# Optimization experiments

Hardware: AMD Instinct MI355X
Metric: run time of the kernel (lower is better)

## Reference

```python
import jax
import jax.numpy as jnp
from jax import lax
import numpy as np

# module hyperparameters (match init_kwargs)
IN_C, OUT_C = 32, 64
K, STRIDE, PAD, DIL = 3, 1, 1, 1
GRID_SIZE, ORDER = 5, 3
GRID_LO, GRID_HI = -1.0, 1.0
SCALE_SPLINE = 1.0
EPS = 1e-8


def _knot_grid():
    # grid = arange(-order, grid_size+order+1) * h + lo ; length = grid_size + 2*order + 1 = 12
    h = (GRID_HI - GRID_LO) / GRID_SIZE
    return jnp.arange(-ORDER, GRID_SIZE + ORDER + 1, dtype=jnp.float32) * h + GRID_LO


def _bspline_bases(x):
    """Cox-de Boor recursion. x: (N, P) -> bases: (N, P, GRID_SIZE+ORDER)."""
    grid = _knot_grid()
    xe = x[..., None]  # (N, P, 1)
    bases = ((xe >= grid[:-1]) & (xe < grid[1:])).astype(x.dtype)  # (N, P, 11)
    for k in range(1, ORDER + 1):
        left_den = jnp.maximum(grid[k:-1] - grid[:-(k + 1)], EPS)
        right_den = jnp.maximum(grid[k + 1:] - grid[1:-k], EPS)
        bases = ((xe - grid[:-(k + 1)]) / left_den * bases[..., :-1]
                 + (grid[k + 1:] - xe) / right_den * bases[..., 1:])
    return bases  # (N, P, 8)


def setup_inputs() -> dict:
    key = jax.random.key(0)
    k1, k2, k3 = jax.random.split(key, 3)
    x = jax.random.normal(k1, (4, IN_C, 56, 56), dtype=jnp.float32)
    base_weight = jax.random.normal(k2, (OUT_C, IN_C, K, K), dtype=jnp.float32) * 0.05
    spline_weight = jax.random.normal(k3, (OUT_C, IN_C * K * K, GRID_SIZE + ORDER), dtype=jnp.float32) * 0.05
    spline_scaler = jnp.ones((OUT_C,), dtype=jnp.float32)
    return {"x": x, "base_weight": base_weight,
            "spline_weight": spline_weight, "spline_scaler": spline_scaler}


def reference(x, base_weight, spline_weight, spline_scaler):
    B, C, H, W = x.shape
    pad = [(PAD, PAD), (PAD, PAD)]
    # base path: conv2d -> SiLU
    base_conv = lax.conv_general_dilated(
        x, base_weight, window_strides=(STRIDE, STRIDE), padding=pad,
        rhs_dilation=(DIL, DIL), dimension_numbers=("NCHW", "OIHW", "NCHW"))
    base_out = jax.nn.silu(base_conv)

    # unfold: (B, C*K*K, oh, ow) with torch Unfold channel ordering (c, kh, kw)
    patches = lax.conv_general_dilated_patches(
        x, filter_shape=(K, K), window_strides=(STRIDE, STRIDE), padding=pad,
        rhs_dilation=(DIL, DIL))
    oh, ow = patches.shape[2], patches.shape[3]
    num_patches = oh * ow
    # (B*num_patches, C*K*K)
    pf = patches.reshape(B, C * K * K, num_patches).transpose(0, 2, 1).reshape(-1, C * K * K)

    bases = _bspline_bases(pf)  # (N, P, F)
    # contract patch-dim and basis-dim against spline weights
    spl = jnp.einsum("npf,opf->no", bases, spline_weight) * spline_scaler  # (N, O)
    spl = spl.reshape(B, num_patches, OUT_C).transpose(0, 2, 1).reshape(B, OUT_C, oh, ow)
    return base_out + SCALE_SPLINE * spl
```

## Files before the change

### kernel.cpp

```cpp
#include <hip/hip_runtime.h>
#include <math.h>


typedef __attribute__((ext_vector_type(8))) short bf16x8;
typedef __attribute__((ext_vector_type(4))) float f32x4;
typedef __attribute__((ext_vector_type(16))) float f32x16;

#define MFMA32(a, b, c) __builtin_amdgcn_mfma_f32_32x32x16_bf16((a), (b), (c), 0, 0, 0)

__device__ __forceinline__ unsigned short f2bf(float f) {
    unsigned u = __builtin_bit_cast(unsigned, f);
    u = (u + 0x7fffu + ((u >> 16) & 1u)) >> 16;
    return (unsigned short)u;
}

__device__ __forceinline__ void eval_bases(float v, float bs[8]) {
    #pragma unroll
    for (int i = 0; i < 8; ++i) bs[i] = 0.0f;
    float t = (v + 2.2f) * 2.5f;
    if (t >= 0.0f && t < 11.0f) {
        int j = (int)t;
        if (j > 10) j = 10;
        float knot = (float)(j - 3) * 0.4f - 1.0f;
        float u  = (v - knot) * 2.5f;
        float um = 1.0f - u;
        float u2 = u * u, u3 = u2 * u;
        const float s6 = 1.0f / 6.0f;
        float w0 = um * um * um * s6;
        float w1 = (3.0f * u3 - 6.0f * u2 + 4.0f) * s6;
        float w2 = (-3.0f * u3 + 3.0f * u2 + 3.0f * u + 1.0f) * s6;
        float w3 = u3 * s6;
        int i0 = j - 3;
        if (i0 >= 0)               bs[i0]     = w0;
        if (i0 + 1 >= 0 && i0 < 7) bs[i0 + 1] = w1;
        if (i0 + 2 >= 0 && i0 < 6) bs[i0 + 2] = w2;
        if (i0 + 3 <= 7)           bs[i0 + 3] = w3;
    }
}

__global__ __launch_bounds__(256)
void cvt_swz_kernel(const float* __restrict__ ws, const float* __restrict__ wb,
                    unsigned short* __restrict__ wst, unsigned short* __restrict__ wbt) {
    int i = blockIdx.x * 256 + threadIdx.x;
    if (i < 147456) {
        int j = i & 7, l = (i >> 3) & 63, tq = i >> 9;
        int t = tq % 144, nqq = tq / 144;
        int oc = nqq * 32 + (l & 31);
        int k  = t * 16 + (l >> 5) * 8 + j;
        wst[i] = f2bf(ws[oc * 2304 + k]);
    } else {
        int i2 = i - 147456;
        if (i2 < 18432) {
            int j = i2 & 7, l = (i2 >> 3) & 63, tq = i2 >> 9;
            int t = tq % 18, nqq = tq / 18;
            int oc  = nqq * 32 + (l & 31);
            int tap = t >> 1;
            int c   = 16 * (t & 1) + (l >> 5) * 8 + j;
            wbt[i2] = f2bf(wb[oc * 288 + c * 9 + tap]);
        }
    }
}

__global__ __launch_bounds__(512)
void kan_mfma_kernel(const float* __restrict__ x,
                     const float* __restrict__ sc,
                     const unsigned short* __restrict__ wst,
                     const unsigned short* __restrict__ wbt,
                     float* __restrict__ out) {
    __shared__ unsigned short smem[29600];
    unsigned short* sb = smem;
    unsigned short* xh = smem + 25600;

    const int tid = threadIdx.x;
    const int bx  = blockIdx.x;
    const int b   = bx / 49;
    const int r   = bx - b * 49;
    const int ty  = r / 7;
    const int tx  = r - ty * 7;
    const int h0  = ty * 8, w0 = tx * 8;

    const int lane = tid & 63;
    const int wv   = tid >> 6;
    const int nqq  = wv & 1;
    const int kq   = wv >> 1;
    const int hl   = lane >> 5;
    const int rl   = lane & 31;
    const int py   = rl >> 3, px = rl & 7;

    float vv[7];
    #pragma unroll
    for (int j = 0; j < 7; ++j) {
        int i = tid + j * 512;
        float val = 0.0f;
        if (i < 3200) {
            int c  = i / 100;
            int hp = i - c * 100;
            int hy = hp / 10;
            int hx = hp - hy * 10;
            int hh = h0 + hy - 1, ww = w0 + hx - 1;
            if ((unsigned)hh < 56u && (unsigned)ww < 56u)
                val = x[((b * 32 + c) * 56 + hh) * 56 + ww];
        }
        vv[j] = val;
    }
    #pragma unroll
    for (int j = 0; j < 7; ++j) {
        int i = tid + j * 512;
        if (i < 3200) {
            int c  = i / 100;
            int hp = i - c * 100;
            float bs[8];
            eval_bases(vv[j], bs);
            bf16x8 pk;
            #pragma unroll
            for (int j2 = 0; j2 < 8; ++j2) pk[j2] = (short)f2bf(bs[j2]);
            *reinterpret_cast<bf16x8*>(&sb[i * 8]) = pk;
            xh[hp * 40 + c] = f2bf(vv[j]);
        }
    }
    __syncthreads();

    int aoff2[9];
    #pragma unroll
    for (int u = 0; u < 9; ++u) {
        int tt  = 2 * u + hl;
        int dc  = tt >= 9 ? 1 : 0;
        int tap = tt - 9 * dc;
        int th  = tap / 3;
        int tw  = tap - th * 3;
        aoff2[u] = (dc * 100 + (py + th) * 10 + (px + tw)) * 8;
    }

    f32x16 accS0 = {0,0,0,0,0,0,0,0,0,0,0,0,0,0,0,0};
    f32x16 accS1 = {0,0,0,0,0,0,0,0,0,0,0,0,0,0,0,0};

    const unsigned short* bp = wst + ((nqq * 144 + kq * 36) * 64 + lane) * 8;
    for (int a = 0; a < 4; ++a) {
        const int cbase = (kq * 8 + 2 * a) * 800;
        #pragma unroll
        for (int u = 0; u < 9; ++u) {
            bf16x8 bw = *reinterpret_cast<const bf16x8*>(bp + (a * 9 + u) * 512);
            bf16x8 a0 = *reinterpret_cast<const bf16x8*>(&sb[cbase + aoff2[u]]);
            bf16x8 a1 = *reinterpret_cast<const bf16x8*>(&sb[cbase + aoff2[u] + 320]);
            accS0 = MFMA32(a0, bw, accS0);
            accS1 = MFMA32(a1, bw, accS1);
        }
    }

    f32x16 accB0 = {0,0,0,0,0,0,0,0,0,0,0,0,0,0,0,0};
    f32x16 accB1 = {0,0,0,0,0,0,0,0,0,0,0,0,0,0,0,0};
    if (kq == 0) {
        const unsigned short* bbp = wbt + (nqq * 18 * 64 + lane) * 8;
        const int c0 = hl * 8;
        #pragma unroll
        for (int t = 0; t < 18; ++t) {
            const int tap = t >> 1, th = tap / 3, tw = tap - 3 * th;
            bf16x8 bw = *reinterpret_cast<const bf16x8*>(bbp + t * 512);
            int xa = ((py + th) * 10 + (px + tw)) * 40 + 16 * (t & 1) + c0;
            bf16x8 a0 = *reinterpret_cast<const bf16x8*>(&xh[xa]);
            bf16x8 a1 = *reinterpret_cast<const bf16x8*>(&xh[xa + 1600]);
            accB0 = MFMA32(a0, bw, accB0);
            accB1 = MFMA32(a1, bw, accB1);
        }
    }

    __syncthreads();
    float* red = reinterpret_cast<float*>(smem);
    const int col = nqq * 64 + lane;
    if (kq) {
        const int rb = (kq - 1) * 4096;
        #pragma unroll
        for (int w = 0; w < 16; ++w) red[rb + w * 128 + col] = accS0[w];
        #pragma unroll
        for (int w = 0; w < 16; ++w) red[rb + (16 + w) * 128 + col] = accS1[w];
    }
    __syncthreads();
    if (kq == 0) {
        #pragma unroll
        for (int rr = 0; rr < 3; ++rr) {
            const int rb = rr * 4096;
            #pragma unroll
            for (int w = 0; w < 16; ++w) accS0[w] += red[rb + w * 128 + col];
            #pragma unroll
            for (int w = 0; w < 16; ++w) accS1[w] += red[rb + (16 + w) * 128 + col];
        }

        const int oc  = nqq * 32 + rl;
        const float scv = sc[oc];
        #pragma unroll
        for (int mq = 0; mq < 2; ++mq) {
            f32x16 aS = mq ? accS1 : accS0;
            f32x16 aB = mq ? accB1 : accB0;
            #pragma unroll
            for (int q = 0; q < 4; ++q) {
                float* ob = out + ((b * 64 + oc) * 56 + h0 + mq * 4 + q) * 56 + w0 + 4 * hl;
                f32x4 res;
                #pragma unroll
                for (int rr = 0; rr < 4; ++rr) {
                    float bv = aB[q * 4 + rr];
                    float si = bv / (1.0f + __expf(-bv));
                    res[rr] = si + scv * aS[q * 4 + rr];
                }
                *reinterpret_cast<f32x4*>(ob) = res;
            }
        }
    }
}

extern "C" void kernel_launch(void* const* d_in, const int* in_sizes, int n_in,
                              void* d_out, int out_size, void* d_ws, size_t ws_size,
                              hipStream_t stream) {
    const float* x  = (const float*)d_in[0];
    const float* wb = (const float*)d_in[1];
    const float* ws = (const float*)d_in[2];
    const float* sc = (const float*)d_in[3];
    float* out = (float*)d_out;

    unsigned short* wst = (unsigned short*)d_ws;
    unsigned short* wbt = wst + 147456;

    cvt_swz_kernel<<<648, 256, 0, stream>>>(ws, wb, wst, wbt);
    kan_mfma_kernel<<<196, 512, 0, stream>>>(x, sc, wst, wbt, out);
}
```

Before: 76.83 us.

## Repartition warps into M-halves and K-halves, prefetch weights into registers

Warps now split the output tile by row-half (mh) and the reduction dimension into two halves (kh), instead of four K-quarters each holding two M-blocks. The base-conv MFMAs are spread over all warps rather than only the kq==0 group, and the LDS cross-warp reduction shrinks from three partials to one. Spline weight fragments are double-buffered in registers and base weights are loaded before the first barrier, so global loads overlap the basis evaluation and the MFMA work. The cost is higher register pressure from the 18-entry weight buffer, plus one extra exchanged accumulator for the base path.

```diff
diff --git a/kernel.cpp b/kernel.cpp
--- a/kernel.cpp
+++ b/kernel.cpp
@@ -82,10 +82,12 @@
     const int lane = tid & 63;
     const int wv   = tid >> 6;
     const int nqq  = wv & 1;
-    const int kq   = wv >> 1;
+    const int kh   = (wv >> 1) & 1;
+    const int mh   = wv >> 2;
+    const int rl   = lane & 31;
     const int hl   = lane >> 5;
-    const int rl   = lane & 31;
-    const int py   = rl >> 3, px = rl & 7;
+    const int py0  = (rl >> 3) + 4 * mh;
+    const int px0  = rl & 7;
 
     float vv[7];
     #pragma unroll
@@ -118,9 +120,24 @@
             xh[hp * 40 + c] = f2bf(vv[j]);
         }
     }
+
+    const unsigned short* bp = wst + ((nqq * 144 + kh * 72) * 64 + lane) * 8;
+    bf16x8 bwbuf[2][9];
+    #pragma unroll
+    for (int u = 0; u < 9; ++u)
+        bwbuf[0][u] = *reinterpret_cast<const bf16x8*>(bp + u * 512);
+
+    bf16x8 bbv[9];
+    {
+        const unsigned short* bbp = wbt + ((nqq * 18 + kh * 9) * 64 + lane) * 8;
+        #pragma unroll
+        for (int s = 0; s < 9; ++s)
+            bbv[s] = *reinterpret_cast<const bf16x8*>(bbp + s * 512);
+    }
+
     __syncthreads();
 
-    int aoff2[9];
+    int aoff[9];
     #pragma unroll
     for (int u = 0; u < 9; ++u) {
         int tt  = 2 * u + hl;
@@ -128,81 +145,69 @@
         int tap = tt - 9 * dc;
         int th  = tap / 3;
         int tw  = tap - th * 3;
-        aoff2[u] = (dc * 100 + (py + th) * 10 + (px + tw)) * 8;
-    }
-
-    f32x16 accS0 = {0,0,0,0,0,0,0,0,0,0,0,0,0,0,0,0};
-    f32x16 accS1 = {0,0,0,0,0,0,0,0,0,0,0,0,0,0,0,0};
-
-    const unsigned short* bp = wst + ((nqq * 144 + kq * 36) * 64 + lane) * 8;
-    for (int a = 0; a < 4; ++a) {
-        const int cbase = (kq * 8 + 2 * a) * 800;
+        aoff[u] = (dc * 100 + (py0 + th) * 10 + (px0 + tw)) * 8;
+    }
+
+    f32x16 accS = {0,0,0,0,0,0,0,0,0,0,0,0,0,0,0,0};
+    f32x16 accB = {0,0,0,0,0,0,0,0,0,0,0,0,0,0,0,0};
+
+    #pragma unroll
+    for (int a = 0; a < 8; ++a) {
+        const int cur = a & 1;
+        if (a < 7) {
+            #pragma unroll
+            for (int u = 0; u < 9; ++u)
+                bwbuf[cur ^ 1][u] =
+                    *reinterpret_cast<const bf16x8*>(bp + ((a + 1) * 9 + u) * 512);
+        }
+        const int cbase = (kh * 16 + 2 * a) * 800;
         #pragma unroll
         for (int u = 0; u < 9; ++u) {
-            bf16x8 bw = *reinterpret_cast<const bf16x8*>(bp + (a * 9 + u) * 512);
-            bf16x8 a0 = *reinterpret_cast<const bf16x8*>(&sb[cbase + aoff2[u]]);
-            bf16x8 a1 = *reinterpret_cast<const bf16x8*>(&sb[cbase + aoff2[u] + 320]);
-            accS0 = MFMA32(a0, bw, accS0);
-            accS1 = MFMA32(a1, bw, accS1);
-        }
-    }
-
-    f32x16 accB0 = {0,0,0,0,0,0,0,0,0,0,0,0,0,0,0,0};
-    f32x16 accB1 = {0,0,0,0,0,0,0,0,0,0,0,0,0,0,0,0};
-    if (kq == 0) {
-        const unsigned short* bbp = wbt + (nqq * 18 * 64 + lane) * 8;
-        const int c0 = hl * 8;
-        #pragma unroll
-        for (int t = 0; t < 18; ++t) {
-            const int tap = t >> 1, th = tap / 3, tw = tap - 3 * th;
-            bf16x8 bw = *reinterpret_cast<const bf16x8*>(bbp + t * 512);
-            int xa = ((py + th) * 10 + (px + tw)) * 40 + 16 * (t & 1) + c0;
-            bf16x8 a0 = *reinterpret_cast<const bf16x8*>(&xh[xa]);
-            bf16x8 a1 = *reinterpret_cast<const bf16x8*>(&xh[xa + 1600]);
-            accB0 = MFMA32(a0, bw, accB0);
-            accB1 = MFMA32(a1, bw, accB1);
-        }
+            bf16x8 av = *reinterpret_cast<const bf16x8*>(&sb[cbase + aoff[u]]);
+            accS = MFMA32(av, bwbuf[cur][u], accS);
+        }
+    }
+
+    #pragma unroll
+    for (int s = 0; s < 9; ++s) {
+        const int t   = kh * 9 + s;
+        const int tap = t >> 1;
+        const int th  = tap >= 6 ? 2 : (tap >= 3 ? 1 : 0);
+        const int tw  = tap - 3 * th;
+        const int xa  = ((py0 + th) * 10 + (px0 + tw)) * 40 + 16 * (t & 1) + hl * 8;
+        bf16x8 av = *reinterpret_cast<const bf16x8*>(&xh[xa]);
+        accB = MFMA32(av, bbv[s], accB);
     }
 
     __syncthreads();
     float* red = reinterpret_cast<float*>(smem);
-    const int col = nqq * 64 + lane;
-    if (kq) {
-        const int rb = (kq - 1) * 4096;
-        #pragma unroll
-        for (int w = 0; w < 16; ++w) red[rb + w * 128 + col] = accS0[w];
-        #pragma unroll
-        for (int w = 0; w < 16; ++w) red[rb + (16 + w) * 128 + col] = accS1[w];
+    const int idx = (mh * 2 + nqq) * 64 + lane;
+    if (kh) {
+        #pragma unroll
+        for (int w = 0; w < 16; ++w) red[w * 260 + idx] = accS[w];
+        #pragma unroll
+        for (int w = 0; w < 16; ++w) red[(16 + w) * 260 + idx] = accB[w];
     }
     __syncthreads();
-    if (kq == 0) {
-        #pragma unroll
-        for (int rr = 0; rr < 3; ++rr) {
-            const int rb = rr * 4096;
-            #pragma unroll
-            for (int w = 0; w < 16; ++w) accS0[w] += red[rb + w * 128 + col];
-            #pragma unroll
-            for (int w = 0; w < 16; ++w) accS1[w] += red[rb + (16 + w) * 128 + col];
-        }
+    if (!kh) {
+        #pragma unroll
+        for (int w = 0; w < 16; ++w) accS[w] += red[w * 260 + idx];
+        #pragma unroll
+        for (int w = 0; w < 16; ++w) accB[w] += red[(16 + w) * 260 + idx];
 
         const int oc  = nqq * 32 + rl;
         const float scv = sc[oc];
         #pragma unroll
-        for (int mq = 0; mq < 2; ++mq) {
-            f32x16 aS = mq ? accS1 : accS0;
-            f32x16 aB = mq ? accB1 : accB0;
+        for (int q = 0; q < 4; ++q) {
+            float* ob = out + ((b * 64 + oc) * 56 + h0 + mh * 4 + q) * 56 + w0 + 4 * hl;
+            f32x4 res;
             #pragma unroll
-            for (int q = 0; q < 4; ++q) {
-                float* ob = out + ((b * 64 + oc) * 56 + h0 + mq * 4 + q) * 56 + w0 + 4 * hl;
-                f32x4 res;
-                #pragma unroll
-                for (int rr = 0; rr < 4; ++rr) {
-                    float bv = aB[q * 4 + rr];
-                    float si = bv / (1.0f + __expf(-bv));
-                    res[rr] = si + scv * aS[q * 4 + rr];
-                }
-                *reinterpret_cast<f32x4*>(ob) = res;
+            for (int rr = 0; rr < 4; ++rr) {
+                float bv = accB[q * 4 + rr];
+                float si = bv / (1.0f + __expf(-bv));
+                res[rr] = si + scv * accS[q * 4 + rr];
             }
+            *reinterpret_cast<f32x4*>(ob) = res;
         }
     }
 }
```

Result: no change. 78.24 us (+1.8%).
